# Optimization experiments

Measured on AMD Instinct MI355X. Metric: run time of the kernel, lower is better.

The kernel has to match this reference:

```python
import jax, jax.numpy as jnp
import numpy as np

PS = 8  # patch_size


def setup_inputs() -> dict:
    key = jax.random.key(0)
    k1, k2 = jax.random.split(key)
    shape = (16, 3, 512, 512)
    return {
        "input": jax.random.normal(k1, shape, dtype=jnp.float32),
        "target": jax.random.normal(k2, shape, dtype=jnp.float32),
    }


def _extract_patches(x):
    # (B,C,H,W) -> (B,C,nh,nw,ps,ps); H,W assumed divisible by PS (no pad needed)
    B, C, H, W = x.shape
    x = x.reshape(B, C, H // PS, PS, W // PS, PS)
    return jnp.transpose(x, (0, 1, 2, 4, 3, 5))


def _fft_feats(patches):
    fft = jnp.fft.fft2(patches, norm="ortho")          # over last two axes
    fft = jnp.fft.fftshift(fft, axes=(-2, -1))
    real, imag = fft.real, fft.imag
    # log1p norm: sign(x) * log1p(|x|)
    real = jnp.sign(real) * jnp.log1p(jnp.abs(real))
    imag = jnp.sign(imag) * jnp.log1p(jnp.abs(imag))
    return real, imag


def reference(input, target):
    ir, ii = _fft_feats(_extract_patches(input))
    tr, ti = _fft_feats(_extract_patches(target))
    loss = (ir - tr) ** 2 + (ii - ti) ** 2   # mse real + mse imag, unreduced
    return jnp.mean(loss)
```

## Files before the change

### kernel.cpp

```cpp
#include <hip/hip_runtime.h>

#define SQ1_2 0.70710678118654752440f

__device__ __forceinline__ float g_feat(float x) {
    return copysignf(__logf(1.0f + fabsf(x)), x);
}

__device__ __forceinline__ void rfft8(const float r[8], float o[8]) {
    float s0 = r[0] + r[4], d0 = r[0] - r[4];
    float s1 = r[1] + r[5], d1 = r[1] - r[5];
    float s2 = r[2] + r[6], d2 = r[2] - r[6];
    float s3 = r[3] + r[7], d3 = r[3] - r[7];
    float ss02 = s0 + s2, sd02 = s0 - s2;
    float ss13 = s1 + s3, sd13 = s1 - s3;
    float t1 = SQ1_2 * (d1 - d3);
    float t2 = SQ1_2 * (d1 + d3);
    o[0] = ss02 + ss13;
    o[1] = ss02 - ss13;
    o[2] = d0 + t1;
    o[3] = -(d2 + t2);
    o[4] = sd02;
    o[5] = -sd13;
    o[6] = d0 - t1;
    o[7] = d2 - t2;
}

__device__ __forceinline__ void cfft8(const float xr[8], const float xi[8],
                                      float Fr[8], float Fi[8]) {
    float s0r = xr[0] + xr[4], s0i = xi[0] + xi[4], d0r = xr[0] - xr[4], d0i = xi[0] - xi[4];
    float s1r = xr[1] + xr[5], s1i = xi[1] + xi[5], d1r = xr[1] - xr[5], d1i = xi[1] - xi[5];
    float s2r = xr[2] + xr[6], s2i = xi[2] + xi[6], d2r = xr[2] - xr[6], d2i = xi[2] - xi[6];
    float s3r = xr[3] + xr[7], s3i = xi[3] + xi[7], d3r = xr[3] - xr[7], d3i = xi[3] - xi[7];
    float ss0r = s0r + s2r, ss0i = s0i + s2i, sd0r = s0r - s2r, sd0i = s0i - s2i;
    float ss1r = s1r + s3r, ss1i = s1i + s3i, sd1r = s1r - s3r, sd1i = s1i - s3i;
    Fr[0] = ss0r + ss1r; Fi[0] = ss0i + ss1i;
    Fr[4] = ss0r - ss1r; Fi[4] = ss0i - ss1i;
    Fr[2] = sd0r + sd1i; Fi[2] = sd0i - sd1r;
    Fr[6] = sd0r - sd1i; Fi[6] = sd0i + sd1r;
    float t1r = SQ1_2 * (d1r + d1i), t1i = SQ1_2 * (d1i - d1r);
    float t2r = d2i,                 t2i = -d2r;
    float t3r = SQ1_2 * (d3i - d3r), t3i = -SQ1_2 * (d3r + d3i);
    float ts0r = d0r + t2r, ts0i = d0i + t2i, td0r = d0r - t2r, td0i = d0i - t2i;
    float ts1r = t1r + t3r, ts1i = t1i + t3i, td1r = t1r - t3r, td1i = t1i - t3i;
    Fr[1] = ts0r + ts1r; Fi[1] = ts0i + ts1i;
    Fr[5] = ts0r - ts1r; Fi[5] = ts0i - ts1i;
    Fr[3] = td0r + td1i; Fi[3] = td0i - td1r;
    Fr[7] = td0r - td1i; Fi[7] = td0i + td1r;
}

__global__ __launch_bounds__(256, 8) void patchfft_stage_kernel(
        const float* __restrict__ in, const float* __restrict__ tgt,
        float* __restrict__ partial) {
    __shared__ float lds[4096];
    __shared__ float wsum[4];
    const int tid = threadIdx.x;

    {
        const int pair = tid >> 3;
        const int T    = (tid >> 2) & 1;
        const int r2   = tid & 3;
        const int p  = blockIdx.x * 32 + pair;
        const int pw = p & 63;
        const int ph = (p >> 6) & 63;
        const int bc = p >> 12;
        const long base = (long)bc * 262144 + ph * 4096 + pw * 8;
        const float* __restrict__ src = T ? tgt : in;
        const int tp = pair * 2 + T;
        const int s  = tp & 7;
        #pragma unroll
        for (int mm = 0; mm < 2; ++mm) {
            const int m = 2 * r2 + mm;
            const float4* p4 = reinterpret_cast<const float4*>(src + base + (long)m * 512);
            float4 a0 = p4[0];
            float4 a1 = p4[1];
            float r[8] = {a0.x * 0.125f, a0.y * 0.125f, a0.z * 0.125f, a0.w * 0.125f,
                          a1.x * 0.125f, a1.y * 0.125f, a1.z * 0.125f, a1.w * 0.125f};
            float o[8];
            rfft8(r, o);
            float4* dst = reinterpret_cast<float4*>(&lds[tp * 64 + ((m ^ s) << 3)]);
            dst[0] = make_float4(o[0], o[1], o[2], o[3]);
            dst[1] = make_float4(o[4], o[5], o[6], o[7]);
        }
    }
    __syncthreads();

    float loss;
    {
        const int pair = tid >> 3;
        const int T    = (tid >> 2) & 1;
        const int task = tid & 3;
        const int tp = pair * 2 + T;
        const int s  = tp & 7;
        float zr[8], zi[8];
        #pragma unroll
        for (int m = 0; m < 8; ++m) {
            float2 z = *reinterpret_cast<const float2*>(
                &lds[tp * 64 + ((m ^ s) << 3) + task * 2]);
            zr[m] = z.x;
            zi[m] = z.y;
        }
        float Fr[8], Fi[8];
        cfft8(zr, zi, Fr, Fi);

        float acc1 = 0.0f, acc2 = 0.0f;
        if (task == 0) {
            float w0 = g_feat(Fr[0]), w1 = g_feat(Fr[4]);
            float w2 = g_feat(Fi[0]), w3 = g_feat(Fi[4]);
            float d0 = w0 - __shfl_xor(w0, 4, 64);
            float d1 = w1 - __shfl_xor(w1, 4, 64);
            float d2 = w2 - __shfl_xor(w2, 4, 64);
            float d3 = w3 - __shfl_xor(w3, 4, 64);
            acc1 = d0 * d0 + d1 * d1 + d2 * d2 + d3 * d3;
            #pragma unroll
            for (int k = 1; k <= 3; ++k) {
                float v0 = 0.5f * (Fr[k] + Fr[8 - k]);
                float v1 = 0.5f * (Fi[k] - Fi[8 - k]);
                float v2 = 0.5f * (Fi[k] + Fi[8 - k]);
                float v3 = 0.5f * (Fr[k] - Fr[8 - k]);
                float f0 = g_feat(v0), f1 = g_feat(v1), f2 = g_feat(v2), f3 = g_feat(v3);
                float e0 = f0 - __shfl_xor(f0, 4, 64);
                float e1 = f1 - __shfl_xor(f1, 4, 64);
                float e2 = f2 - __shfl_xor(f2, 4, 64);
                float e3 = f3 - __shfl_xor(f3, 4, 64);
                acc2 += e0 * e0 + e1 * e1 + e2 * e2 + e3 * e3;
            }
        } else {
            #pragma unroll
            for (int k = 0; k < 8; ++k) {
                float fr = g_feat(Fr[k]);
                float fi = g_feat(Fi[k]);
                float dr = fr - __shfl_xor(fr, 4, 64);
                float di = fi - __shfl_xor(fi, 4, 64);
                acc2 += dr * dr + di * di;
            }
        }
        loss = acc1 + 2.0f * acc2;
    }

    #pragma unroll
    for (int off = 32; off > 0; off >>= 1) loss += __shfl_down(loss, off, 64);
    if ((tid & 63) == 0) wsum[tid >> 6] = loss;
    __syncthreads();
    if (tid == 0) {
        atomicAdd(&partial[blockIdx.x & 255], wsum[0] + wsum[1] + wsum[2] + wsum[3]);
    }
}

__global__ void patchfft_final_kernel(const float* __restrict__ partial,
                                      float* __restrict__ out) {
    float s = partial[threadIdx.x] + partial[threadIdx.x + 64]
            + partial[threadIdx.x + 128] + partial[threadIdx.x + 192];
    #pragma unroll
    for (int off = 32; off > 0; off >>= 1) s += __shfl_down(s, off, 64);
    if (threadIdx.x == 0) *out = s * (1.0f / 25165824.0f);
}

extern "C" void kernel_launch(void* const* d_in, const int* in_sizes, int n_in,
                              void* d_out, int out_size, void* d_ws, size_t ws_size,
                              hipStream_t stream) {
    const float* in  = (const float*)d_in[0];
    const float* tgt = (const float*)d_in[1];
    float* out = (float*)d_out;
    float* partial = (float*)d_ws;
    (void)in_sizes; (void)n_in; (void)ws_size; (void)out_size;

    hipMemsetAsync(partial, 0, 256 * sizeof(float), stream);
    patchfft_stage_kernel<<<6144, 256, 0, stream>>>(in, tgt, partial);
    patchfft_final_kernel<<<1, 64, 0, stream>>>(partial, out);
}
```

Measured before the change: 124.4 us.

## Stage raw patch rows into LDS via global_load_lds before row FFTs

Replaces the per-thread strided float4 global loads with wave-wide async global-to-LDS copies (global_load_lds) of contiguous 1 KB row chunks. Row FFTs then read from padded LDS instead of global memory, and spectra go into a separate padded region in place of the XOR-swizzled layout. LDS usage roughly doubles, so launch bounds drop from 8 to 4 blocks per CU. This reduces occupancy and adds an extra barrier in exchange for fully coalesced DMA-style loads.

```diff
diff --git a/kernel.cpp b/kernel.cpp
--- a/kernel.cpp
+++ b/kernel.cpp
@@ -1,6 +1,12 @@
 #include <hip/hip_runtime.h>
+#include <stdint.h>
 
 #define SQ1_2 0.70710678118654752440f
+
+#define RAW_CHUNK 264
+#define SPEC_OFF  4224
+#define SPEC_REC  68
+#define LDS_FLOATS 8576
 
 __device__ __forceinline__ float g_feat(float x) {
     return copysignf(__logf(1.0f + fabsf(x)), x);
@@ -48,36 +54,57 @@
     Fr[7] = td0r - td1i; Fi[7] = td0i + td1r;
 }
 
-__global__ __launch_bounds__(256, 8) void patchfft_stage_kernel(
+__global__ __launch_bounds__(256, 4) void patchfft_stage_kernel(
         const float* __restrict__ in, const float* __restrict__ tgt,
         float* __restrict__ partial) {
-    __shared__ float lds[4096];
+    __shared__ float lds[LDS_FLOATS];
     __shared__ float wsum[4];
     const int tid = threadIdx.x;
 
     {
-        const int pair = tid >> 3;
-        const int T    = (tid >> 2) & 1;
-        const int r2   = tid & 3;
-        const int p  = blockIdx.x * 32 + pair;
-        const int pw = p & 63;
-        const int ph = (p >> 6) & 63;
-        const int bc = p >> 12;
-        const long base = (long)bc * 262144 + ph * 4096 + pw * 8;
-        const float* __restrict__ src = T ? tgt : in;
-        const int tp = pair * 2 + T;
-        const int s  = tp & 7;
+        const int w    = tid >> 6;
+        const int lane = tid & 63;
+        const int p0 = blockIdx.x * 32;
+        const int pw0 = p0 & 63;
+        const int ph  = (p0 >> 6) & 63;
+        const int bc  = p0 >> 12;
+        const long gbase = (long)bc * 262144 + (long)ph * 4096 + pw0 * 8;
+        #pragma unroll
+        for (int i = 0; i < 4; ++i) {
+            const int k = w * 4 + i;
+            const int T = k >> 3;
+            const int m = k & 7;
+            const float* src = T ? tgt : in;
+            const float* gp = src + gbase + (long)m * 512 + lane * 4;
+            __builtin_amdgcn_global_load_lds(
+                (const __attribute__((address_space(1))) void*)gp,
+                (__attribute__((address_space(3))) void*)&lds[k * RAW_CHUNK],
+                16, 0, 0);
+        }
+    }
+    __syncthreads();
+
+    const int pw = tid >> 3;
+    const int T  = (tid >> 2) & 1;
+    const int rec = SPEC_OFF + (pw * 2 + T) * SPEC_REC;
+
+    {
+        const int r2 = tid & 3;
         #pragma unroll
         for (int mm = 0; mm < 2; ++mm) {
             const int m = 2 * r2 + mm;
-            const float4* p4 = reinterpret_cast<const float4*>(src + base + (long)m * 512);
-            float4 a0 = p4[0];
-            float4 a1 = p4[1];
-            float r[8] = {a0.x * 0.125f, a0.y * 0.125f, a0.z * 0.125f, a0.w * 0.125f,
-                          a1.x * 0.125f, a1.y * 0.125f, a1.z * 0.125f, a1.w * 0.125f};
+            const int rb = (T * 8 + m) * RAW_CHUNK + pw * 8;
+            float r[8];
+            #pragma unroll
+            for (int j = 0; j < 4; ++j) {
+                const int c = (r2 + j) & 3;
+                float2 z = *reinterpret_cast<const float2*>(&lds[rb + c * 2]);
+                r[c * 2]     = z.x * 0.125f;
+                r[c * 2 + 1] = z.y * 0.125f;
+            }
             float o[8];
             rfft8(r, o);
-            float4* dst = reinterpret_cast<float4*>(&lds[tp * 64 + ((m ^ s) << 3)]);
+            float4* dst = reinterpret_cast<float4*>(&lds[rec + m * 8]);
             dst[0] = make_float4(o[0], o[1], o[2], o[3]);
             dst[1] = make_float4(o[4], o[5], o[6], o[7]);
         }
@@ -86,16 +113,11 @@
 
     float loss;
     {
-        const int pair = tid >> 3;
-        const int T    = (tid >> 2) & 1;
         const int task = tid & 3;
-        const int tp = pair * 2 + T;
-        const int s  = tp & 7;
         float zr[8], zi[8];
         #pragma unroll
         for (int m = 0; m < 8; ++m) {
-            float2 z = *reinterpret_cast<const float2*>(
-                &lds[tp * 64 + ((m ^ s) << 3) + task * 2]);
+            float2 z = *reinterpret_cast<const float2*>(&lds[rec + m * 8 + task * 2]);
             zr[m] = z.x;
             zi[m] = z.y;
         }
```

New measurement: 134.3 us. 1.08x slower.
